# Performance work log

Hardware: AMD Instinct MI355X
Metric: run time of the kernel (lower is better)

The kernel has to match this reference:

```python
import jax, jax.numpy as jnp
import numpy as np

EPS = 1e-5  # nn.LayerNorm default

def _ln(x, g, b):
    m = x.mean(-1, keepdims=True)
    v = ((x - m) ** 2).mean(-1, keepdims=True)
    return (x - m) / jnp.sqrt(v + EPS) * g + b


def setup_inputs() -> dict:
    key = jax.random.key(0)
    ks = jax.random.split(key, 16)
    B, T, H, W = 8, 20, 224, 224
    D, NC = 1536, 7
    s = 0.02
    f32 = jnp.float32
    return {
        'x': jax.random.normal(ks[0], (B, 3, T, H, W), f32),
        'timestamp': jax.random.uniform(ks[1], (B,), f32),
        # surrogate backbone: patchify conv (stride 16) + global avg pool -> 1536 feats
        'conv_w': jax.random.normal(ks[2], (D, 3, 16, 16), f32) * s,
        'conv_b': jnp.zeros((D,), f32),
        'w_red': jax.random.normal(ks[3], (D, D), f32) * s,
        'b_red': jnp.zeros((D,), f32),
        'w_num': jax.random.normal(ks[4], (D, 1), f32) * s,
        'b_num': jnp.zeros((D,), f32),
        'time_embed': jax.random.normal(ks[5], (1, T, D), f32) * s,
        'cls_swap': jax.random.normal(ks[6], (1, 5, 1, D), f32) * s,
        'ln_g': jnp.ones((D,), f32),
        'ln_b': jnp.zeros((D,), f32),
        'w_qkv': jax.random.normal(ks[7], (3 * D, D), f32) * s,
        'w_tproj': jax.random.normal(ks[8], (D, D), f32) * s,
        'b_tproj': jnp.zeros((D,), f32),
        'w_tfc': jax.random.normal(ks[9], (D, D), f32) * s,
        'b_tfc': jnp.zeros((D,), f32),
        'w_head': jax.random.normal(ks[10], (NC, D), f32) * s,
        'b_head': jnp.zeros((NC,), f32),
    }


def reference(x, timestamp, conv_w, conv_b, w_red, b_red, w_num, b_num,
              time_embed, cls_swap, ln_g, ln_b, w_qkv, w_tproj, b_tproj,
              w_tfc, b_tfc, w_head, b_head):
    B, C, T, H, W = x.shape
    D = w_red.shape[0]
    NH = 12
    HD = D // NH
    scale = HD ** -0.5

    # (b t) c h w  -> backbone surrogate -> (B*T, D)
    xf = jnp.transpose(x, (0, 2, 1, 3, 4)).reshape(B * T, C, H, W)
    f = jax.lax.conv_general_dilated(
        xf, conv_w, window_strides=(16, 16), padding='VALID',
        dimension_numbers=('NCHW', 'OIHW', 'NCHW'))
    f = (f + conv_b[None, :, None, None]).mean((2, 3))  # global avg pool -> (BT, D)

    xr = (f @ w_red.T + b_red).reshape(B, T, D)           # reduce_dim
    xt = xr + time_embed
    te = timestamp[:, None] @ w_num.T + b_num             # NumberToVector (B, D)
    xt = xt + te[:, None, :]

    # groups: b (n k) c -> b n k c, k=4, n=5; prepend 1 cls token per group
    g = jnp.concatenate(
        [jnp.broadcast_to(cls_swap, (B, 5, 1, D)), xt.reshape(B, 5, 4, D)], axis=2)

    for _ in range(4):  # num_interactions
        gr = g.reshape(B * 5, 5, D)
        hn = _ln(gr, ln_g, ln_b)
        qkv = (hn @ w_qkv.T).reshape(B * 5, 5, 3, NH, HD).transpose(2, 0, 3, 1, 4)
        q, k, v = qkv[0], qkv[1], qkv[2]                  # (b*n, h, t, hd)
        a = jax.nn.softmax(jnp.einsum('bhqd,bhkd->bhqk', q, k) * scale, axis=-1)
        o = jnp.einsum('bhqk,bhkd->bhqd', a, v).transpose(0, 2, 1, 3).reshape(B * 5, 5, D)
        o = o @ w_tproj.T + b_tproj                       # attn proj
        upd = (o @ w_tfc.T + b_tfc) + gr                  # temporal_fc + residual
        g = upd.reshape(B, 5, 5, D)
        # swap cls tokens between groups via roll
        g = g.at[:, :, 0, :].set(jnp.roll(g[:, :, 0, :], 1, axis=1))

    xt = g[:, :, 1:, :].reshape(B, T, D)
    out = xt[:, -1, :] + xr[:, -1, :]
    return out @ w_head.T + b_head  # (B, num_classes)
```

## Files before the change

kernel.cpp:

```cpp
#include <hip/hip_runtime.h>

typedef __attribute__((ext_vector_type(8))) short short8;
typedef __attribute__((ext_vector_type(8))) unsigned short ushort8;
typedef __attribute__((ext_vector_type(4))) float f32x4;
typedef unsigned short ushort_t;

__device__ __forceinline__ ushort_t f2bf(float f) {
    unsigned u = __builtin_bit_cast(unsigned, f);
    u += 0x7fffu + ((u >> 16) & 1u);
    return (ushort_t)(u >> 16);
}

__device__ __forceinline__ void load_lds16(const void* gp, void* lp) {
    __builtin_amdgcn_global_load_lds(
        (const __attribute__((address_space(1))) void*)gp,
        (__attribute__((address_space(3))) void*)lp, 16, 0, 0);
}

__global__ __launch_bounds__(256, 4) void pool_kernel(
    const float* __restrict__ x, ushort_t* __restrict__ AP) {
    int blk = blockIdx.x, tid = threadIdx.x;
    int bt = blk / 12, rc = blk % 12;
    int c = rc >> 2, igrp = rc & 3;
    int w = tid >> 6, lane = tid & 63;
    int i = igrp * 4 + w;
    int b = bt / 20, t = bt % 20;
    const float* base = x + (size_t)((b * 3 + c) * 20 + t) * 50176;

    f32x4 v[13];
    #pragma unroll
    for (int it = 0; it < 13; ++it) {
        int k = lane + it * 64;
        int kk = k < 784 ? k : 0;
        int ri = (kk * 9363) >> 19;
        int c4 = kk - ri * 56;
        v[it] = *(const f32x4*)(base + (16 * ri + i) * 224 + 4 * c4);
        if (k >= 784) v[it] = (f32x4){0.f, 0.f, 0.f, 0.f};
    }
    #pragma unroll
    for (int s = 1; s < 13; s <<= 1)
        #pragma unroll
        for (int j = 0; j + s < 13; j += 2 * s)
            v[j] += v[j + s];
    f32x4 acc = v[0];
    #pragma unroll
    for (int m = 4; m <= 32; m <<= 1) {
        acc[0] += __shfl_xor(acc[0], m);
        acc[1] += __shfl_xor(acc[1], m);
        acc[2] += __shfl_xor(acc[2], m);
        acc[3] += __shfl_xor(acc[3], m);
    }
    if (lane < 4) {
        ushort4 o;
        o.x = f2bf(acc[0] * (1.f / 196.f));
        o.y = f2bf(acc[1] * (1.f / 196.f));
        o.z = f2bf(acc[2] * (1.f / 196.f));
        o.w = f2bf(acc[3] * (1.f / 196.f));
        *(ushort4*)(AP + (size_t)bt * 768 + c * 256 + i * 16 + 4 * lane) = o;
    }
}

__global__ __launch_bounds__(256) void wprep_kernel(
    const float* __restrict__ w_qkv, const float* __restrict__ w_tf,
    const float* __restrict__ w_red, const float* __restrict__ conv_w,
    const float* __restrict__ w_tp, const float* __restrict__ b_tp,
    const float* __restrict__ b_tf, const float* __restrict__ conv_b,
    const float* __restrict__ b_red, const float* __restrict__ cls,
    ushort_t* __restrict__ WQ, ushort_t* __restrict__ WF,
    ushort_t* __restrict__ WR, ushort_t* __restrict__ WCVT,
    ushort_t* __restrict__ WTT, float* __restrict__ BC,
    float* __restrict__ BC2, float* __restrict__ GA) {
    __shared__ __align__(16) float smem[64 * 68];
    int blk = blockIdx.x, tid = threadIdx.x;
    if (blk < 5760) {
        long c = (long)blk * 256 + tid;
        const float* s; ushort_t* d; long i;
        if (c < 884736)       { s = w_qkv; d = WQ; i = c; }
        else if (c < 1179648) { s = w_tf;  d = WF; i = c - 884736; }
        else                  { s = w_red; d = WR; i = c - 1179648; }
        i <<= 3;
        f32x4 a = *(const f32x4*)(s + i);
        f32x4 b = *(const f32x4*)(s + i + 4);
        ushort8 o;
        o[0] = f2bf(a[0]); o[1] = f2bf(a[1]); o[2] = f2bf(a[2]); o[3] = f2bf(a[3]);
        o[4] = f2bf(b[0]); o[5] = f2bf(b[1]); o[6] = f2bf(b[2]); o[7] = f2bf(b[3]);
        *(ushort8*)(d + i) = o;
    } else if (blk < 6336) {
        int tb = blk - 5760;
        int bi = tb / 24, bj = tb % 24;
        int r0 = (tid >> 4) << 2;
        int c0 = (tid & 15) << 2;
        #pragma unroll
        for (int rr = 0; rr < 4; ++rr) {
            f32x4 v = *(const f32x4*)(w_tp + (size_t)(bi * 64 + r0 + rr) * 1536 + bj * 64 + c0);
            smem[(r0 + rr) * 68 + c0 + 0] = v[0];
            smem[(r0 + rr) * 68 + c0 + 1] = v[1];
            smem[(r0 + rr) * 68 + c0 + 2] = v[2];
            smem[(r0 + rr) * 68 + c0 + 3] = v[3];
        }
        __syncthreads();
        #pragma unroll
        for (int rr = 0; rr < 4; ++rr) {
            int jj = r0 + rr;
            ushort4 o;
            o.x = f2bf(smem[(c0 + 0) * 68 + jj]);
            o.y = f2bf(smem[(c0 + 1) * 68 + jj]);
            o.z = f2bf(smem[(c0 + 2) * 68 + jj]);
            o.w = f2bf(smem[(c0 + 3) * 68 + jj]);
            *(ushort4*)(WTT + (size_t)(bj * 64 + jj) * 1536 + bi * 64 + c0) = o;
        }
    } else if (blk < 6624) {
        int tb = blk - 6336;
        int bi = tb / 12, bj = tb % 12;
        int r0 = (tid >> 4) << 2;
        int c0 = (tid & 15) << 2;
        #pragma unroll
        for (int rr = 0; rr < 4; ++rr) {
            f32x4 v = *(const f32x4*)(conv_w + (size_t)(bi * 64 + r0 + rr) * 768 + bj * 64 + c0);
            smem[(r0 + rr) * 68 + c0 + 0] = v[0];
            smem[(r0 + rr) * 68 + c0 + 1] = v[1];
            smem[(r0 + rr) * 68 + c0 + 2] = v[2];
            smem[(r0 + rr) * 68 + c0 + 3] = v[3];
        }
        __syncthreads();
        #pragma unroll
        for (int rr = 0; rr < 4; ++rr) {
            int jj = r0 + rr;
            ushort4 o;
            o.x = f2bf(smem[(c0 + 0) * 68 + jj]);
            o.y = f2bf(smem[(c0 + 1) * 68 + jj]);
            o.z = f2bf(smem[(c0 + 2) * 68 + jj]);
            o.w = f2bf(smem[(c0 + 3) * 68 + jj]);
            *(ushort4*)(WCVT + (size_t)(bj * 64 + jj) * 1536 + bi * 64 + c0) = o;
        }
    } else if (blk < 6664) {
        int cblk = blk - 6624;
        int b = cblk / 5, n = cblk % 5;
        size_t row = (size_t)(b * 25 + n * 5) * 1536;
        #pragma unroll
        for (int j = 0; j < 6; ++j) {
            int d = tid + j * 256;
            GA[row + d] = cls[n * 1536 + d];
        }
    } else if (blk < 6760) {
        int bb = blk - 6664;
        int row = bb * 16 + (tid >> 4);
        int sub = tid & 15;
        float acc = 0.f;
        for (int j = 0; j < 96; ++j) {
            int k = sub + j * 16;
            acc += w_tf[(size_t)row * 1536 + k] * b_tp[k];
        }
        acc += __shfl_xor(acc, 1); acc += __shfl_xor(acc, 2);
        acc += __shfl_xor(acc, 4); acc += __shfl_xor(acc, 8);
        if (sub == 0) BC[row] = acc + b_tf[row];
    } else {
        int bb = blk - 6760;
        int row = bb * 16 + (tid >> 4);
        int sub = tid & 15;
        float acc = 0.f;
        for (int j = 0; j < 48; ++j) {
            int n0 = sub + j * 16;
            acc += w_red[(size_t)row * 1536 + n0] * conv_b[n0];
            acc += w_red[(size_t)row * 1536 + n0 + 768] * conv_b[n0 + 768];
        }
        acc += __shfl_xor(acc, 1); acc += __shfl_xor(acc, 2);
        acc += __shfl_xor(acc, 4); acc += __shfl_xor(acc, 8);
        if (sub == 0) BC2[row] = acc + b_red[row];
    }
}

template <bool OUT_BF16>
__device__ __forceinline__ void gemm128_tile(
    char* lds, const ushort_t* __restrict__ A, const ushort_t* __restrict__ B,
    void* __restrict__ Cv, int M, int N, int K, int KS, int tn, int tm) {
    const int tid = threadIdx.x;
    const int lane = tid & 63;
    const int w = tid >> 6;
    const int wr = w >> 1, wc = w & 1;

    f32x4 acc[4][4];
    #pragma unroll
    for (int m = 0; m < 4; ++m)
        #pragma unroll
        for (int n = 0; n < 4; ++n)
            acc[m][n] = (f32x4){0.f, 0.f, 0.f, 0.f};

    const int nK = K >> 6;
    const int rbase = lane >> 3, cc = lane & 7;

    auto stage = [&](int k0, int buf) {
        char* lA = lds + buf * 32768;
        char* lB = lA + 16384;
        #pragma unroll
        for (int j = 0; j < 4; ++j) {
            int row = w * 32 + j * 8 + rbase;
            int cf = cc ^ (row & 7);
            int ga = tm * 128 + row; if (ga > M - 1) ga = M - 1;
            load_lds16(A + (size_t)ga * KS + (k0 + cf * 8),
                       lA + (w * 32 + j * 8) * 128);
        }
        #pragma unroll
        for (int j = 0; j < 4; ++j) {
            int row = w * 32 + j * 8 + rbase;
            int cf = cc ^ (row & 7);
            load_lds16(B + (size_t)(tn * 128 + row) * KS + (k0 + cf * 8),
                       lB + (w * 32 + j * 8) * 128);
        }
    };

    stage(0, 0);
    asm volatile("s_waitcnt vmcnt(0)" ::: "memory");
    __builtin_amdgcn_s_barrier();
    __builtin_amdgcn_sched_barrier(0);
    for (int t = 0; t < nK; ++t) {
        int cur = t & 1;
        if (t + 1 < nK) stage((t + 1) << 6, cur ^ 1);
        __builtin_amdgcn_sched_barrier(0);
        const char* lA = lds + cur * 32768;
        const char* lB = lA + 16384;
        #pragma unroll
        for (int ks = 0; ks < 2; ++ks) {
            short8 av[4], bv[4];
            const int rlo = lane & 15;
            const int chi = ks * 4 + (lane >> 4);
            #pragma unroll
            for (int m = 0; m < 4; ++m) {
                int r = wr * 64 + m * 16 + rlo;
                av[m] = *(const short8*)(lA + r * 128 + ((chi ^ (r & 7)) << 4));
            }
            #pragma unroll
            for (int n = 0; n < 4; ++n) {
                int r = wc * 64 + n * 16 + rlo;
                bv[n] = *(const short8*)(lB + r * 128 + ((chi ^ (r & 7)) << 4));
            }
            #pragma unroll
            for (int m = 0; m < 4; ++m)
                #pragma unroll
                for (int n = 0; n < 4; ++n)
                    acc[m][n] = __builtin_amdgcn_mfma_f32_16x16x32_bf16(
                        av[m], bv[n], acc[m][n], 0, 0, 0);
        }
        asm volatile("s_waitcnt vmcnt(0)" ::: "memory");
        __builtin_amdgcn_s_barrier();
        __builtin_amdgcn_sched_barrier(0);
    }

    const int c_l = lane & 15, r_q = (lane >> 4) * 4;
    #pragma unroll
    for (int m = 0; m < 4; ++m) {
        #pragma unroll
        for (int reg = 0; reg < 4; ++reg) {
            int r_ = tm * 128 + wr * 64 + m * 16 + r_q + reg;
            if (r_ < M) {
                #pragma unroll
                for (int n = 0; n < 4; ++n) {
                    int cc_ = tn * 128 + wc * 64 + n * 16 + c_l;
                    float v = acc[m][n][reg];
                    if (OUT_BF16) ((ushort_t*)Cv)[(size_t)r_ * N + cc_] = f2bf(v);
                    else          ((float*)Cv)[(size_t)r_ * N + cc_] = v;
                }
            }
        }
    }
}

__global__ __launch_bounds__(256) void wcf_kernel(
    const ushort_t* __restrict__ WF, const ushort_t* __restrict__ WTT,
    const ushort_t* __restrict__ WR, const ushort_t* __restrict__ WCVT,
    ushort_t* __restrict__ WC, ushort_t* __restrict__ WRC) {
    __shared__ __align__(16) char lds[65536];
    int task = blockIdx.x;
    if (task < 144)
        gemm128_tile<true>(lds, WF, WTT, WC, 1536, 1536, 1536, 1536,
                           task % 12, task / 12);
    else {
        int t2 = task - 144;
        gemm128_tile<true>(lds, WR, WCVT, WRC, 1536, 768, 1536, 1536,
                           t2 % 6, t2 / 6);
    }
}

__global__ __launch_bounds__(256) void qkv_kernel(
    const ushort_t* __restrict__ HN, const ushort_t* __restrict__ WQ,
    float* __restrict__ C0, float* __restrict__ C1) {
    __shared__ __align__(16) char lds[65536];
    int tn = blockIdx.x, y = blockIdx.y;
    int half = y >> 1, tm = y & 1;
    gemm128_tile<false>(lds, HN + half * 768, WQ + half * 768,
                        half ? C1 : C0, 200, 4608, 768, 1536, tn, tm);
}

template <int MT, bool OUT_BF16, bool HAS_BIAS, bool HAS_RES, bool CLS_SWAP, bool BUILD_G>
__device__ __forceinline__ void gemm_tile(
    char* lds, int lane, int tn, int tm,
    const ushort_t* __restrict__ A, const ushort_t* __restrict__ B,
    void* __restrict__ Cv, const float* __restrict__ bias,
    const float* __restrict__ res, int M, int N, int K, int KS,
    float* __restrict__ g_out, const float* __restrict__ temb,
    const float* __restrict__ ts, const float* __restrict__ w_num,
    const float* __restrict__ b_num) {
    constexpr int BUFB = MT * 2048 + 8192;

    f32x4 acc[MT][4];
    #pragma unroll
    for (int m = 0; m < MT; ++m)
        #pragma unroll
        for (int n = 0; n < 4; ++n)
            acc[m][n] = (f32x4){0.f, 0.f, 0.f, 0.f};

    const int nK = K >> 6;
    const int rbase = lane >> 3, cc = lane & 7;

    auto stage = [&](int k0, int buf) {
        char* lA = lds + buf * BUFB;
        char* lB = lA + MT * 2048;
        #pragma unroll
        for (int j = 0; j < MT * 2; ++j) {
            int row = j * 8 + rbase;
            int cf = cc ^ (row & 7);
            int ga = tm * (MT * 16) + row; if (ga > M - 1) ga = M - 1;
            load_lds16(A + (size_t)ga * KS + (k0 + cf * 8), lA + j * 1024);
        }
        #pragma unroll
        for (int j = 0; j < 8; ++j) {
            int row = j * 8 + rbase;
            int cf = cc ^ (row & 7);
            load_lds16(B + (size_t)(tn * 64 + row) * KS + (k0 + cf * 8), lB + j * 1024);
        }
    };

    stage(0, 0);
    for (int t = 0; t < nK; ++t) {
        int cur = t & 1;
        if (t + 1 < nK) {
            stage((t + 1) << 6, cur ^ 1);
            if constexpr (MT == 2) asm volatile("s_waitcnt vmcnt(12)" ::: "memory");
            else                   asm volatile("s_waitcnt vmcnt(16)" ::: "memory");
        } else {
            asm volatile("s_waitcnt vmcnt(0)" ::: "memory");
        }
        __builtin_amdgcn_sched_barrier(0);
        const char* lA = lds + cur * BUFB;
        const char* lB = lA + MT * 2048;
        #pragma unroll
        for (int ks = 0; ks < 2; ++ks) {
            short8 av[MT], bv[4];
            const int rlo = lane & 15;
            const int chi = ks * 4 + (lane >> 4);
            #pragma unroll
            for (int m = 0; m < MT; ++m) {
                int r = m * 16 + rlo;
                av[m] = *(const short8*)(lA + r * 128 + ((chi ^ (r & 7)) << 4));
            }
            #pragma unroll
            for (int n = 0; n < 4; ++n) {
                int r = n * 16 + rlo;
                bv[n] = *(const short8*)(lB + r * 128 + ((chi ^ (r & 7)) << 4));
            }
            #pragma unroll
            for (int m = 0; m < MT; ++m)
                #pragma unroll
                for (int n = 0; n < 4; ++n)
                    acc[m][n] = __builtin_amdgcn_mfma_f32_16x16x32_bf16(
                        av[m], bv[n], acc[m][n], 0, 0, 0);
        }
    }

    const int c_l = lane & 15, r_q = (lane >> 4) * 4;
    #pragma unroll
    for (int m = 0; m < MT; ++m) {
        #pragma unroll
        for (int reg = 0; reg < 4; ++reg) {
            int r_ = tm * (MT * 16) + m * 16 + r_q + reg;
            if (r_ < M) {
                int r2 = r_;
                if (CLS_SWAP) {
                    int bb = r_ / 25, rem = r_ % 25;
                    if (rem % 5 == 0) r2 = bb * 25 + ((rem / 5 + 1) % 5) * 5;
                }
                #pragma unroll
                for (int n = 0; n < 4; ++n) {
                    int cc_ = tn * 64 + n * 16 + c_l;
                    float v = acc[m][n][reg];
                    if (HAS_BIAS) v += bias[cc_];
                    if (HAS_RES) v += res[(size_t)r_ * N + cc_];
                    if (OUT_BF16) ((ushort_t*)Cv)[(size_t)r2 * N + cc_] = f2bf(v);
                    else          ((float*)Cv)[(size_t)r2 * N + cc_] = v;
                    if (BUILD_G) {
                        int b = r_ / 20, t = r_ % 20;
                        float gval = v + temb[t * 1536 + cc_] +
                                     ts[b] * w_num[cc_] + b_num[cc_];
                        g_out[(size_t)(b * 25 + (t / 4) * 5 + (t % 4) + 1) * 1536 + cc_] = gval;
                    }
                }
            }
        }
    }
}

__global__ __launch_bounds__(64) void xr_kernel(
    const ushort_t* __restrict__ AP, const ushort_t* __restrict__ WRC,
    float* __restrict__ XR, const float* __restrict__ BC2,
    float* __restrict__ GA, const float* __restrict__ temb,
    const float* __restrict__ ts, const float* __restrict__ w_num,
    const float* __restrict__ b_num) {
    __shared__ __align__(16) char lds[24576];
    gemm_tile<2, false, true, false, false, true>(
        lds, threadIdx.x, blockIdx.x, blockIdx.y, AP, WRC, XR, BC2, nullptr,
        160, 1536, 768, 768, GA, temb, ts, w_num, b_num);
}

__global__ __launch_bounds__(64) void proj_kernel(
    const ushort_t* __restrict__ OBF, const ushort_t* __restrict__ WC,
    float* __restrict__ gdst, const float* __restrict__ BC,
    const float* __restrict__ gsrc) {
    __shared__ __align__(16) char lds[24576];
    gemm_tile<2, false, true, true, true, false>(
        lds, threadIdx.x, blockIdx.x, blockIdx.y, OBF, WC, gdst, BC, gsrc,
        200, 1536, 1536, 1536, nullptr, nullptr, nullptr, nullptr, nullptr);
}

__global__ __launch_bounds__(256) void ln_kernel(
    const float* __restrict__ g, const float* __restrict__ gamma,
    const float* __restrict__ beta, ushort_t* __restrict__ hn) {
    int r = blockIdx.x, tid = threadIdx.x;
    const float* x = g + (size_t)r * 1536;
    float v[6], s = 0.f, s2 = 0.f;
    #pragma unroll
    for (int j = 0; j < 6; ++j) {
        v[j] = x[tid + j * 256];
        s += v[j]; s2 += v[j] * v[j];
    }
    #pragma unroll
    for (int m = 1; m < 64; m <<= 1) { s += __shfl_xor(s, m); s2 += __shfl_xor(s2, m); }
    __shared__ float red[8];
    int wid = tid >> 6;
    if ((tid & 63) == 0) { red[wid] = s; red[4 + wid] = s2; }
    __syncthreads();
    s  = red[0] + red[1] + red[2] + red[3];
    s2 = red[4] + red[5] + red[6] + red[7];
    float mean = s * (1.0f / 1536.0f);
    float var  = s2 * (1.0f / 1536.0f) - mean * mean;
    float rstd = rsqrtf(var + 1e-5f);
    #pragma unroll
    for (int j = 0; j < 6; ++j) {
        int d = tid + j * 256;
        float y = (v[j] - mean) * rstd * gamma[d] + beta[d];
        hn[(size_t)r * 1536 + d] = f2bf(y);
    }
}

__global__ __launch_bounds__(64) void attn_kernel(
    const float* __restrict__ qA, const float* __restrict__ qB,
    ushort_t* __restrict__ o) {
    int gid = blockIdx.x;
    int h = gid % 12, gg = gid / 12;
    int l = threadIdx.x;
    size_t off = (size_t)gg * 5 * 4608 + h * 128 + 2 * l;
    const float* b0 = qA + off;
    const float* b1 = qB + off;
    float q[5][2], k[5][2], v[5][2];
    #pragma unroll
    for (int tt = 0; tt < 5; ++tt) {
        float2 q0 = *(const float2*)(b0 + tt * 4608);
        float2 q1 = *(const float2*)(b1 + tt * 4608);
        float2 k0 = *(const float2*)(b0 + tt * 4608 + 1536);
        float2 k1 = *(const float2*)(b1 + tt * 4608 + 1536);
        float2 v0 = *(const float2*)(b0 + tt * 4608 + 3072);
        float2 v1 = *(const float2*)(b1 + tt * 4608 + 3072);
        q[tt][0] = q0.x + q1.x; q[tt][1] = q0.y + q1.y;
        k[tt][0] = k0.x + k1.x; k[tt][1] = k0.y + k1.y;
        v[tt][0] = v0.x + v1.x; v[tt][1] = v0.y + v1.y;
    }
    float sc[5][5];
    #pragma unroll
    for (int i = 0; i < 5; ++i)
        #pragma unroll
        for (int j = 0; j < 5; ++j)
            sc[i][j] = q[i][0] * k[j][0] + q[i][1] * k[j][1];
    #pragma unroll
    for (int m = 1; m < 64; m <<= 1)
        #pragma unroll
        for (int i = 0; i < 5; ++i)
            #pragma unroll
            for (int j = 0; j < 5; ++j)
                sc[i][j] += __shfl_xor(sc[i][j], m);
    const float scale = 0.08838834764831845f;
    float a_[5][5];
    #pragma unroll
    for (int i = 0; i < 5; ++i) {
        float mx = -1e30f;
        #pragma unroll
        for (int j = 0; j < 5; ++j) mx = fmaxf(mx, sc[i][j]);
        float sum = 0.f;
        #pragma unroll
        for (int j = 0; j < 5; ++j) { a_[i][j] = __expf((sc[i][j] - mx) * scale); sum += a_[i][j]; }
        float inv = 1.0f / sum;
        #pragma unroll
        for (int j = 0; j < 5; ++j) a_[i][j] *= inv;
    }
    #pragma unroll
    for (int i = 0; i < 5; ++i) {
        float o0 = 0.f, o1 = 0.f;
        #pragma unroll
        for (int j = 0; j < 5; ++j) { o0 += a_[i][j] * v[j][0]; o1 += a_[i][j] * v[j][1]; }
        ushort2 w; w.x = f2bf(o0); w.y = f2bf(o1);
        *(ushort2*)(o + (size_t)(gg * 5 + i) * 1536 + h * 128 + 2 * l) = w;
    }
}

__global__ __launch_bounds__(64) void head_kernel(
    const float* __restrict__ gfin, const float* __restrict__ xr,
    const float* __restrict__ w_head, const float* __restrict__ b_head,
    float* __restrict__ out) {
    int b = blockIdx.x, l = threadIdx.x;
    const float* gv = gfin + (size_t)(b * 25 + 24) * 1536;
    const float* xv = xr + (size_t)(b * 20 + 19) * 1536;
    float acc[7] = {0, 0, 0, 0, 0, 0, 0};
    for (int d = l; d < 1536; d += 64) {
        float xval = gv[d] + xv[d];
        #pragma unroll
        for (int c = 0; c < 7; ++c) acc[c] += xval * w_head[c * 1536 + d];
    }
    #pragma unroll
    for (int c = 0; c < 7; ++c)
        #pragma unroll
        for (int m = 1; m < 64; m <<= 1) acc[c] += __shfl_xor(acc[c], m);
    if (l == 0) {
        #pragma unroll
        for (int c = 0; c < 7; ++c) out[b * 7 + c] = acc[c] + b_head[c];
    }
}

#define OFF_WQ    0u
#define OFF_WF    14155776u
#define OFF_WR    18874368u
#define OFF_WCVT  23592960u
#define OFF_WTT   25952256u
#define OFF_WC    30670848u
#define OFF_WRC   35389440u
#define OFF_BC    37748736u
#define OFF_BC2   37754880u
#define OFF_AP    37761024u
#define OFF_XR    38006784u
#define OFF_GA    38989824u
#define OFF_GB    40218624u
#define OFF_HN    41447424u
#define OFF_QKV0  42061824u
#define OFF_QKV1  45748224u
#define OFF_OBF   49434624u

extern "C" void kernel_launch(void* const* d_in, const int* in_sizes, int n_in,
                              void* d_out, int out_size, void* d_ws, size_t ws_size,
                              hipStream_t stream) {
    const float* x      = (const float*)d_in[0];
    const float* ts     = (const float*)d_in[1];
    const float* conv_w = (const float*)d_in[2];
    const float* conv_b = (const float*)d_in[3];
    const float* w_red  = (const float*)d_in[4];
    const float* b_red  = (const float*)d_in[5];
    const float* w_num  = (const float*)d_in[6];
    const float* b_num  = (const float*)d_in[7];
    const float* temb   = (const float*)d_in[8];
    const float* cls    = (const float*)d_in[9];
    const float* ln_g   = (const float*)d_in[10];
    const float* ln_b   = (const float*)d_in[11];
    const float* w_qkv  = (const float*)d_in[12];
    const float* w_tp   = (const float*)d_in[13];
    const float* b_tp   = (const float*)d_in[14];
    const float* w_tf   = (const float*)d_in[15];
    const float* b_tf   = (const float*)d_in[16];
    const float* w_head = (const float*)d_in[17];
    const float* b_head = (const float*)d_in[18];

    char* ws = (char*)d_ws;
    ushort_t* WQ   = (ushort_t*)(ws + OFF_WQ);
    ushort_t* WF   = (ushort_t*)(ws + OFF_WF);
    ushort_t* WR   = (ushort_t*)(ws + OFF_WR);
    ushort_t* WCVT = (ushort_t*)(ws + OFF_WCVT);
    ushort_t* WTT  = (ushort_t*)(ws + OFF_WTT);
    ushort_t* WC   = (ushort_t*)(ws + OFF_WC);
    ushort_t* WRC  = (ushort_t*)(ws + OFF_WRC);
    float*    BC   = (float*)(ws + OFF_BC);
    float*    BC2  = (float*)(ws + OFF_BC2);
    ushort_t* AP   = (ushort_t*)(ws + OFF_AP);
    float*    XR   = (float*)(ws + OFF_XR);
    float*    GA   = (float*)(ws + OFF_GA);
    float*    GB   = (float*)(ws + OFF_GB);
    ushort_t* HN   = (ushort_t*)(ws + OFF_HN);
    float*    QKV0 = (float*)(ws + OFF_QKV0);
    float*    QKV1 = (float*)(ws + OFF_QKV1);
    ushort_t* OBF  = (ushort_t*)(ws + OFF_OBF);

    pool_kernel<<<1920, 256, 0, stream>>>(x, AP);
    wprep_kernel<<<6856, 256, 0, stream>>>(w_qkv, w_tf, w_red, conv_w, w_tp,
                                           b_tp, b_tf, conv_b, b_red, cls,
                                           WQ, WF, WR, WCVT, WTT, BC, BC2, GA);
    wcf_kernel<<<216, 256, 0, stream>>>(WF, WTT, WR, WCVT, WC, WRC);
    xr_kernel<<<dim3(24, 5), 64, 0, stream>>>(AP, WRC, XR, BC2, GA,
                                              temb, ts, w_num, b_num);
    float* gsrc = GA;
    float* gdst = GB;
    for (int it = 0; it < 4; ++it) {
        ln_kernel<<<200, 256, 0, stream>>>(gsrc, ln_g, ln_b, HN);
        qkv_kernel<<<dim3(36, 4), 256, 0, stream>>>(HN, WQ, QKV0, QKV1);
        attn_kernel<<<480, 64, 0, stream>>>(QKV0, QKV1, OBF);
        proj_kernel<<<dim3(24, 7), 64, 0, stream>>>(OBF, WC, gdst, BC, gsrc);
        float* tmp = gsrc; gsrc = gdst; gdst = tmp;
    }
    head_kernel<<<8, 64, 0, stream>>>(gsrc, XR, w_head, b_head, (float*)d_out);
}
```

Baseline: 207.7 us.

## Merge pool and weight-prep kernels; retile QKV GEMM into more single-wave blocks

Folds the pooling kernel into the weight-prep kernel so both run in one launch, letting the memory-bound input read overlap with weight conversion and removing one launch boundary. The QKV projection moves from the 128x128 gemm128_tile (144 blocks of 256 threads) to the single-wave gemm_tile<4> path with a 72x8 grid of 64-thread blocks. This aims to spread the small-M GEMM over more CUs. In exchange, each block gets less reuse and the merged prep kernel now runs under launch_bounds(256,4) for all of its branches.

Result: faster. 200.5 us (-3.4%).

```diff
diff --git a/kernel.cpp b/kernel.cpp
--- a/kernel.cpp
+++ b/kernel.cpp
@@ -17,63 +17,60 @@
         (__attribute__((address_space(3))) void*)lp, 16, 0, 0);
 }
 
-__global__ __launch_bounds__(256, 4) void pool_kernel(
-    const float* __restrict__ x, ushort_t* __restrict__ AP) {
-    int blk = blockIdx.x, tid = threadIdx.x;
-    int bt = blk / 12, rc = blk % 12;
-    int c = rc >> 2, igrp = rc & 3;
-    int w = tid >> 6, lane = tid & 63;
-    int i = igrp * 4 + w;
-    int b = bt / 20, t = bt % 20;
-    const float* base = x + (size_t)((b * 3 + c) * 20 + t) * 50176;
-
-    f32x4 v[13];
-    #pragma unroll
-    for (int it = 0; it < 13; ++it) {
-        int k = lane + it * 64;
-        int kk = k < 784 ? k : 0;
-        int ri = (kk * 9363) >> 19;
-        int c4 = kk - ri * 56;
-        v[it] = *(const f32x4*)(base + (16 * ri + i) * 224 + 4 * c4);
-        if (k >= 784) v[it] = (f32x4){0.f, 0.f, 0.f, 0.f};
-    }
-    #pragma unroll
-    for (int s = 1; s < 13; s <<= 1)
-        #pragma unroll
-        for (int j = 0; j + s < 13; j += 2 * s)
-            v[j] += v[j + s];
-    f32x4 acc = v[0];
-    #pragma unroll
-    for (int m = 4; m <= 32; m <<= 1) {
-        acc[0] += __shfl_xor(acc[0], m);
-        acc[1] += __shfl_xor(acc[1], m);
-        acc[2] += __shfl_xor(acc[2], m);
-        acc[3] += __shfl_xor(acc[3], m);
-    }
-    if (lane < 4) {
-        ushort4 o;
-        o.x = f2bf(acc[0] * (1.f / 196.f));
-        o.y = f2bf(acc[1] * (1.f / 196.f));
-        o.z = f2bf(acc[2] * (1.f / 196.f));
-        o.w = f2bf(acc[3] * (1.f / 196.f));
-        *(ushort4*)(AP + (size_t)bt * 768 + c * 256 + i * 16 + 4 * lane) = o;
-    }
-}
-
-__global__ __launch_bounds__(256) void wprep_kernel(
-    const float* __restrict__ w_qkv, const float* __restrict__ w_tf,
-    const float* __restrict__ w_red, const float* __restrict__ conv_w,
-    const float* __restrict__ w_tp, const float* __restrict__ b_tp,
-    const float* __restrict__ b_tf, const float* __restrict__ conv_b,
-    const float* __restrict__ b_red, const float* __restrict__ cls,
-    ushort_t* __restrict__ WQ, ushort_t* __restrict__ WF,
-    ushort_t* __restrict__ WR, ushort_t* __restrict__ WCVT,
-    ushort_t* __restrict__ WTT, float* __restrict__ BC,
-    float* __restrict__ BC2, float* __restrict__ GA) {
+__global__ __launch_bounds__(256, 4) void prep_kernel(
+    const float* __restrict__ x, const float* __restrict__ w_qkv,
+    const float* __restrict__ w_tf, const float* __restrict__ w_red,
+    const float* __restrict__ conv_w, const float* __restrict__ w_tp,
+    const float* __restrict__ b_tp, const float* __restrict__ b_tf,
+    const float* __restrict__ conv_b, const float* __restrict__ b_red,
+    const float* __restrict__ cls,
+    ushort_t* __restrict__ AP, ushort_t* __restrict__ WQ,
+    ushort_t* __restrict__ WF, ushort_t* __restrict__ WR,
+    ushort_t* __restrict__ WCVT, ushort_t* __restrict__ WTT,
+    float* __restrict__ BC, float* __restrict__ BC2,
+    float* __restrict__ GA) {
     __shared__ __align__(16) float smem[64 * 68];
     int blk = blockIdx.x, tid = threadIdx.x;
-    if (blk < 5760) {
-        long c = (long)blk * 256 + tid;
+    if (blk < 1920) {
+        int bt = blk / 12, rc = blk % 12;
+        int c = rc >> 2, igrp = rc & 3;
+        int w = tid >> 6, lane = tid & 63;
+        int i = igrp * 4 + w;
+        int b = bt / 20, t = bt % 20;
+        const float* base = x + (size_t)((b * 3 + c) * 20 + t) * 50176;
+        f32x4 v[13];
+        #pragma unroll
+        for (int it = 0; it < 13; ++it) {
+            int k = lane + it * 64;
+            int kk = k < 784 ? k : 0;
+            int ri = (kk * 9363) >> 19;
+            int c4 = kk - ri * 56;
+            v[it] = *(const f32x4*)(base + (16 * ri + i) * 224 + 4 * c4);
+            if (k >= 784) v[it] = (f32x4){0.f, 0.f, 0.f, 0.f};
+        }
+        #pragma unroll
+        for (int s = 1; s < 13; s <<= 1)
+            #pragma unroll
+            for (int j = 0; j + s < 13; j += 2 * s)
+                v[j] += v[j + s];
+        f32x4 acc = v[0];
+        #pragma unroll
+        for (int m = 4; m <= 32; m <<= 1) {
+            acc[0] += __shfl_xor(acc[0], m);
+            acc[1] += __shfl_xor(acc[1], m);
+            acc[2] += __shfl_xor(acc[2], m);
+            acc[3] += __shfl_xor(acc[3], m);
+        }
+        if (lane < 4) {
+            ushort4 o;
+            o.x = f2bf(acc[0] * (1.f / 196.f));
+            o.y = f2bf(acc[1] * (1.f / 196.f));
+            o.z = f2bf(acc[2] * (1.f / 196.f));
+            o.w = f2bf(acc[3] * (1.f / 196.f));
+            *(ushort4*)(AP + (size_t)bt * 768 + c * 256 + i * 16 + 4 * lane) = o;
+        }
+    } else if (blk < 7680) {
+        long c = (long)(blk - 1920) * 256 + tid;
         const float* s; ushort_t* d; long i;
         if (c < 884736)       { s = w_qkv; d = WQ; i = c; }
         else if (c < 1179648) { s = w_tf;  d = WF; i = c - 884736; }
@@ -85,8 +82,8 @@
         o[0] = f2bf(a[0]); o[1] = f2bf(a[1]); o[2] = f2bf(a[2]); o[3] = f2bf(a[3]);
         o[4] = f2bf(b[0]); o[5] = f2bf(b[1]); o[6] = f2bf(b[2]); o[7] = f2bf(b[3]);
         *(ushort8*)(d + i) = o;
-    } else if (blk < 6336) {
-        int tb = blk - 5760;
+    } else if (blk < 8256) {
+        int tb = blk - 7680;
         int bi = tb / 24, bj = tb % 24;
         int r0 = (tid >> 4) << 2;
         int c0 = (tid & 15) << 2;
@@ -109,8 +106,8 @@
             o.w = f2bf(smem[(c0 + 3) * 68 + jj]);
             *(ushort4*)(WTT + (size_t)(bj * 64 + jj) * 1536 + bi * 64 + c0) = o;
         }
-    } else if (blk < 6624) {
-        int tb = blk - 6336;
+    } else if (blk < 8544) {
+        int tb = blk - 8256;
         int bi = tb / 12, bj = tb % 12;
         int r0 = (tid >> 4) << 2;
         int c0 = (tid & 15) << 2;
@@ -133,8 +130,8 @@
             o.w = f2bf(smem[(c0 + 3) * 68 + jj]);
             *(ushort4*)(WCVT + (size_t)(bj * 64 + jj) * 1536 + bi * 64 + c0) = o;
         }
-    } else if (blk < 6664) {
-        int cblk = blk - 6624;
+    } else if (blk < 8584) {
+        int cblk = blk - 8544;
         int b = cblk / 5, n = cblk % 5;
         size_t row = (size_t)(b * 25 + n * 5) * 1536;
         #pragma unroll
@@ -142,8 +139,8 @@
             int d = tid + j * 256;
             GA[row + d] = cls[n * 1536 + d];
         }
-    } else if (blk < 6760) {
-        int bb = blk - 6664;
+    } else if (blk < 8680) {
+        int bb = blk - 8584;
         int row = bb * 16 + (tid >> 4);
         int sub = tid & 15;
         float acc = 0.f;
@@ -155,7 +152,7 @@
         acc += __shfl_xor(acc, 4); acc += __shfl_xor(acc, 8);
         if (sub == 0) BC[row] = acc + b_tf[row];
     } else {
-        int bb = blk - 6760;
+        int bb = blk - 8680;
         int row = bb * 16 + (tid >> 4);
         int sub = tid & 15;
         float acc = 0.f;
@@ -279,16 +276,6 @@
         gemm128_tile<true>(lds, WR, WCVT, WRC, 1536, 768, 1536, 1536,
                            t2 % 6, t2 / 6);
     }
-}
-
-__global__ __launch_bounds__(256) void qkv_kernel(
-    const ushort_t* __restrict__ HN, const ushort_t* __restrict__ WQ,
-    float* __restrict__ C0, float* __restrict__ C1) {
-    __shared__ __align__(16) char lds[65536];
-    int tn = blockIdx.x, y = blockIdx.y;
-    int half = y >> 1, tm = y & 1;
-    gemm128_tile<false>(lds, HN + half * 768, WQ + half * 768,
-                        half ? C1 : C0, 200, 4608, 768, 1536, tn, tm);
 }
 
 template <int MT, bool OUT_BF16, bool HAS_BIAS, bool HAS_RES, bool CLS_SWAP, bool BUILD_G>
@@ -411,6 +398,18 @@
         160, 1536, 768, 768, GA, temb, ts, w_num, b_num);
 }
 
+__global__ __launch_bounds__(64) void qkv_kernel(
+    const ushort_t* __restrict__ HN, const ushort_t* __restrict__ WQ,
+    float* __restrict__ C0, float* __restrict__ C1) {
+    __shared__ __align__(16) char lds[32768];
+    int tn = blockIdx.x, tmh = blockIdx.y;
+    int half = tmh >> 2, tm = tmh & 3;
+    gemm_tile<4, false, false, false, false, false>(
+        lds, threadIdx.x, tn, tm, HN + half * 768, WQ + half * 768,
+        half ? C1 : C0, nullptr, nullptr, 200, 4608, 768, 1536,
+        nullptr, nullptr, nullptr, nullptr, nullptr);
+}
+
 __global__ __launch_bounds__(64) void proj_kernel(
     const ushort_t* __restrict__ OBF, const ushort_t* __restrict__ WC,
     float* __restrict__ gdst, const float* __restrict__ BC,
@@ -593,10 +592,9 @@
     float*    QKV1 = (float*)(ws + OFF_QKV1);
     ushort_t* OBF  = (ushort_t*)(ws + OFF_OBF);
 
-    pool_kernel<<<1920, 256, 0, stream>>>(x, AP);
-    wprep_kernel<<<6856, 256, 0, stream>>>(w_qkv, w_tf, w_red, conv_w, w_tp,
-                                           b_tp, b_tf, conv_b, b_red, cls,
-                                           WQ, WF, WR, WCVT, WTT, BC, BC2, GA);
+    prep_kernel<<<8776, 256, 0, stream>>>(x, w_qkv, w_tf, w_red, conv_w, w_tp,
+                                          b_tp, b_tf, conv_b, b_red, cls,
+                                          AP, WQ, WF, WR, WCVT, WTT, BC, BC2, GA);
     wcf_kernel<<<216, 256, 0, stream>>>(WF, WTT, WR, WCVT, WC, WRC);
     xr_kernel<<<dim3(24, 5), 64, 0, stream>>>(AP, WRC, XR, BC2, GA,
                                               temb, ts, w_num, b_num);
@@ -604,7 +602,7 @@
     float* gdst = GB;
     for (int it = 0; it < 4; ++it) {
         ln_kernel<<<200, 256, 0, stream>>>(gsrc, ln_g, ln_b, HN);
-        qkv_kernel<<<dim3(36, 4), 256, 0, stream>>>(HN, WQ, QKV0, QKV1);
+        qkv_kernel<<<dim3(72, 8), 64, 0, stream>>>(HN, WQ, QKV0, QKV1);
         attn_kernel<<<480, 64, 0, stream>>>(QKV0, QKV1, OBF);
         proj_kernel<<<dim3(24, 7), 64, 0, stream>>>(OBF, WC, gdst, BC, gsrc);
         float* tmp = gsrc; gsrc = gdst; gdst = tmp;
```
